# Kernel tuning notes

Hardware: AMD Instinct MI355X
Metric: run time of the kernel (lower is better)

Reference implementation:

```python
import jax, jax.numpy as jnp
import numpy as np

N = 32768        # nodes
E = 524288       # edges (avg in-degree 16)
G = 256          # graphs in batch (128 nodes each)
D = 64           # hidden_dim
DE = 64          # edge_dim
L = 4            # PNA layers
ATOM, BOND = 32, 8
AVG_D_LOG = float(np.log(17.0))   # avg_d['log'] for avg degree 16
EPS = 1e-5


def setup_inputs() -> dict:
    key = jax.random.key(0)
    ks = jax.random.split(key, 16)
    h_tok = jax.random.randint(ks[0], (N,), 0, ATOM, dtype=jnp.int32)
    e_tok = jax.random.randint(ks[1], (E,), 0, BOND, dtype=jnp.int32)
    src = jax.random.randint(ks[2], (E,), 0, N, dtype=jnp.int32)
    dst = jax.random.randint(ks[3], (E,), 0, N, dtype=jnp.int32)
    graph_id = (jnp.arange(N, dtype=jnp.int32) // (N // G)).astype(jnp.int32)
    snorm_n = jnp.full((N, 1), 1.0 / np.sqrt(N // G), dtype=jnp.float32)
    s = 0.05
    emb_h = s * jax.random.normal(ks[4], (ATOM, D), dtype=jnp.float32)
    emb_e = s * jax.random.normal(ks[5], (BOND, DE), dtype=jnp.float32)
    W_pre = s * jax.random.normal(ks[6], (L, 2 * D + DE, D), dtype=jnp.float32)
    b_pre = jnp.zeros((L, D), dtype=jnp.float32)
    W_post = s * jax.random.normal(ks[7], (L, 13 * D, D), dtype=jnp.float32)
    b_post = jnp.zeros((L, D), dtype=jnp.float32)
    bn_gamma = jnp.ones((L, D), dtype=jnp.float32)
    bn_beta = jnp.zeros((L, D), dtype=jnp.float32)
    W1 = s * jax.random.normal(ks[8], (D, D // 2), dtype=jnp.float32)
    b1 = jnp.zeros((D // 2,), dtype=jnp.float32)
    W2 = s * jax.random.normal(ks[9], (D // 2, D // 4), dtype=jnp.float32)
    b2 = jnp.zeros((D // 4,), dtype=jnp.float32)
    W3 = s * jax.random.normal(ks[10], (D // 4, 1), dtype=jnp.float32)
    b3 = jnp.zeros((1,), dtype=jnp.float32)
    return dict(h_tok=h_tok, e_tok=e_tok, src=src, dst=dst, graph_id=graph_id,
                snorm_n=snorm_n, emb_h=emb_h, emb_e=emb_e,
                W_pre=W_pre, b_pre=b_pre, W_post=W_post, b_post=b_post,
                bn_gamma=bn_gamma, bn_beta=bn_beta,
                W1=W1, b1=b1, W2=W2, b2=b2, W3=W3, b3=b3)


def _pna_forward(h_tok, e_tok, src, dst, graph_id, snorm_n, emb_h, emb_e,
                 W_pre, b_pre, W_post, b_post, bn_gamma, bn_beta,
                 W1, b1, W2, b2, W3, b3):
    h = emb_h[h_tok]                     # [N, D] atom embedding (dropout p=0)
    e = emb_e[e_tok]                     # [E, DE] bond embedding
    deg = jax.ops.segment_sum(jnp.ones((E,), h.dtype), dst, num_segments=N)   # in-degree
    deg_safe = jnp.maximum(deg, 1.0)[:, None]
    logd = jnp.log(deg + 1.0)
    amp = (logd / AVG_D_LOG)[:, None]                        # amplification scaler
    att = (AVG_D_LOG / jnp.maximum(logd, 1e-6))[:, None]     # attenuation scaler
    has_nb = (deg > 0)[:, None]

    for l in range(L):
        h_in = h
        # pretrans on (h_src, h_dst, e)
        m_in = jnp.concatenate([h[src], h[dst], e], axis=-1)          # [E, 2D+DE]
        msg = m_in @ W_pre[l] + b_pre[l]                              # [E, D]
        s1 = jax.ops.segment_sum(msg, dst, num_segments=N)
        s2 = jax.ops.segment_sum(msg * msg, dst, num_segments=N)
        mean = s1 / deg_safe
        std = jnp.sqrt(jax.nn.relu(s2 / deg_safe - mean * mean) + EPS)
        mx = jnp.where(has_nb, jax.ops.segment_max(msg, dst, num_segments=N), 0.0)
        mn = jnp.where(has_nb, jax.ops.segment_min(msg, dst, num_segments=N), 0.0)
        agg = jnp.concatenate([mean, mx, mn, std], axis=-1)           # [N, 4D]
        agg = jnp.concatenate([agg, agg * amp, agg * att], axis=-1)   # [N, 12D]
        # posttrans on (h, aggregated)
        h = jnp.concatenate([h, agg], axis=-1) @ W_post[l] + b_post[l]  # [N, D]
        h = h * snorm_n                                               # graph norm
        mu = jnp.mean(h, axis=0)                                      # batchnorm (train mode)
        var = jnp.var(h, axis=0)
        h = bn_gamma[l] * (h - mu) * jax.lax.rsqrt(var + EPS) + bn_beta[l]
        h = jax.nn.relu(h)
        h = h + h_in                                                  # residual

    # mean-nodes readout per graph
    cnt = jax.ops.segment_sum(jnp.ones((N,), h.dtype), graph_id, num_segments=G)
    hg = jax.ops.segment_sum(h, graph_id, num_segments=G) / jnp.maximum(cnt, 1.0)[:, None]
    # MLPReadout: D -> D/2 -> D/4 -> 1
    out = jax.nn.relu(hg @ W1 + b1)
    out = jax.nn.relu(out @ W2 + b2)
    return out @ W3 + b3                                              # [G, 1]


def reference(h_tok, e_tok, src, dst, graph_id, snorm_n, emb_h, emb_e,
              W_pre, b_pre, W_post, b_post, bn_gamma, bn_beta,
              W1, b1, W2, b2, W3, b3):
    return _pna_forward(h_tok, e_tok, src, dst, graph_id, snorm_n, emb_h, emb_e,
                        W_pre, b_pre, W_post, b_post, bn_gamma, bn_beta,
                        W1, b1, W2, b2, W3, b3)
```

## Files before the change

kernel.cpp:

```cpp
#include <hip/hip_runtime.h>
#include <math.h>
#include <float.h>

#define NN 32768
#define NE 524288
#define NG 256
#define DD 64
#define NL 4
#define AVGDLOG 2.8332133340562162f
#define BN_EPS 1e-5f

typedef __attribute__((ext_vector_type(8))) short bf16x8;
typedef __attribute__((ext_vector_type(4))) float f32x4;

static __device__ __forceinline__ unsigned int f2bf_pack(float lo, float hi) {
    unsigned int ulo = __float_as_uint(lo);
    unsigned int uhi = __float_as_uint(hi);
    ulo = ulo + 0x7FFFu + ((ulo >> 16) & 1u);
    uhi = uhi + 0x7FFFu + ((uhi >> 16) & 1u);
    return (ulo >> 16) | (uhi & 0xFFFF0000u);
}
static __device__ __forceinline__ unsigned short f2bf1(float x) {
    unsigned int u = __float_as_uint(x);
    u = u + 0x7FFFu + ((u >> 16) & 1u);
    return (unsigned short)(u >> 16);
}
static __device__ __forceinline__ float bf2f(unsigned short s) {
    return __uint_as_float((unsigned int)s << 16);
}


__global__ void k_deg(const int* __restrict__ dst, int* __restrict__ deg) {
    int e = blockIdx.x * 256 + threadIdx.x;
    if (e < NE) atomicAdd(&deg[dst[e]], 1);
}

__global__ __launch_bounds__(1024) void k_scan(const int* __restrict__ deg,
                                               int* __restrict__ row_start,
                                               int* __restrict__ cursor,
                                               float* __restrict__ amp,
                                               float* __restrict__ att,
                                               float* __restrict__ invdeg) {
    __shared__ int sd[1024];
    int t = threadIdx.x;
    int base = t * 32;
    int loc[32];
    int s = 0;
#pragma unroll
    for (int i = 0; i < 32; i++) { loc[i] = deg[base + i]; s += loc[i]; }
    sd[t] = s;
    __syncthreads();
    for (int off = 1; off < 1024; off <<= 1) {
        int v = (t >= off) ? sd[t - off] : 0;
        __syncthreads();
        sd[t] += v;
        __syncthreads();
    }
    int run = sd[t] - s;
#pragma unroll
    for (int i = 0; i < 32; i++) {
        int idx = base + i;
        row_start[idx] = run;
        cursor[idx] = run;
        int dg = loc[i];
        float d = (float)dg;
        float logd = logf(d + 1.0f);
        amp[idx] = logd * (1.0f / AVGDLOG);
        att[idx] = AVGDLOG / fmaxf(logd, 1e-6f);
        invdeg[idx] = 1.0f / fmaxf(d, 1.0f);
        run += dg;
    }
    if (t == 1023) row_start[NN] = run;
}

__global__ void k_scatter(const int* __restrict__ src, const int* __restrict__ dst,
                          const int* __restrict__ e_tok, int* __restrict__ cursor,
                          int* __restrict__ csr) {
    int e = blockIdx.x * 256 + threadIdx.x;
    int d = dst[e];
    int p = atomicAdd(&cursor[d], 1);
    csr[p] = (src[e] << 3) | (e_tok[e] & 7);
}

__global__ void k_bond(const float* __restrict__ emb_e, const float* __restrict__ W_pre,
                       const float* __restrict__ b_pre, float* __restrict__ bond) {
    int t = blockIdx.x * 256 + threadIdx.x;
    int j = t & 63, r = (t >> 6) & 7, l = t >> 9;
    float s = b_pre[l * DD + j];
    const float* w = W_pre + (size_t)l * 192 * DD + 128 * DD + j;
    const float* e = emb_e + r * DD;
#pragma unroll
    for (int k = 0; k < DD; k++) s = fmaf(e[k], w[k * DD], s);
    bond[t] = s;
}

__global__ __launch_bounds__(256) void k_wprep(const float* __restrict__ W_post,
                                               unsigned short* __restrict__ wt_hi) {
    int b = blockIdx.x;
    int t = threadIdx.x;
    int l = b / 192;
    int j = b - l * 192;
    int c = j >> 6, jj = j & 63;
    float wv = W_post[((size_t)l * 832 + 64 + c * 256 + t) * 64 + jj];
    wt_hi[((size_t)b << 8) + t] = f2bf1(wv);
}


#define FMA4(acc, a, wv) \
    acc.x = fmaf(a, wv.x, acc.x); acc.y = fmaf(a, wv.y, acc.y); \
    acc.z = fmaf(a, wv.z, acc.z); acc.w = fmaf(a, wv.w, acc.w);

__global__ __launch_bounds__(256) void k_A(const int* __restrict__ h_tok,
                                           const float* __restrict__ emb_h,
                                           const float* __restrict__ h_pre,
                                           float* __restrict__ h_cur,
                                           const float* __restrict__ bn_acc,
                                           const float* __restrict__ gamma,
                                           const float* __restrict__ beta,
                                           const float* __restrict__ W_pre,
                                           const float* __restrict__ W_post, int l,
                                           unsigned short* __restrict__ tsb,
                                           float* __restrict__ td,
                                           float* __restrict__ base_o) {
    __shared__ float wl[3 * 4096];
    __shared__ float hl[64 * 68];
    int t = threadIdx.x;
    int j0 = (t & 15) << 2;
    int q4 = (t >> 4) << 2;
    int n0 = blockIdx.x * 64;
    const float* W0 = W_pre + (size_t)l * 192 * DD;
    const float* W1 = W0 + 64 * DD;
    const float* W2 = W_post + (size_t)l * 832 * DD;
#pragma unroll
    for (int s = 0; s < 12; ++s) {
        int g = s * 256 + t;
        int c = g >> 10;
        int k = (g >> 4) & 63;
        int c4 = (g & 15) << 2;
        const float* Wc = (c == 0) ? W0 : (c == 1 ? W1 : W2);
        *(float4*)&wl[c * 4096 + k * 64 + c4] = *(const float4*)&Wc[(size_t)k * 64 + c4];
    }
    if (l == 0) {
#pragma unroll
        for (int s = 0; s < 4; ++s) {
            int g = s * 256 + t;
            int row = g >> 4;
            int tok = h_tok[n0 + row];
            float4 v = *(const float4*)&emb_h[(size_t)tok * DD + j0];
            *(float4*)&hl[row * 68 + j0] = v;
            *(float4*)&h_cur[(size_t)(n0 + row) * DD + j0] = v;
        }
    } else {
        int lp = l - 1;
        float mu0, mu1, mu2, mu3, iv0, iv1, iv2, iv3;
        float ga0, ga1, ga2, ga3, be0, be1, be2, be3;
#define BNPAR(I, MU, IV, GA, BE) { \
        float m_ = bn_acc[lp * 128 + j0 + I] * (1.0f / NN); \
        float v_ = bn_acc[lp * 128 + 64 + j0 + I] * (1.0f / NN) - m_ * m_; \
        MU = m_; IV = rsqrtf(v_ + BN_EPS); \
        GA = gamma[lp * DD + j0 + I]; BE = beta[lp * DD + j0 + I]; }
        BNPAR(0, mu0, iv0, ga0, be0)
        BNPAR(1, mu1, iv1, ga1, be1)
        BNPAR(2, mu2, iv2, ga2, be2)
        BNPAR(3, mu3, iv3, ga3, be3)
#undef BNPAR
#pragma unroll
        for (int s = 0; s < 4; ++s) {
            int g = s * 256 + t;
            int row = g >> 4;
            size_t gb = (size_t)(n0 + row) * DD + j0;
            float4 hp = *(const float4*)&h_pre[gb];
            float4 hc = *(const float4*)&h_cur[gb];
            float4 v;
            v.x = hc.x + fmaxf(ga0 * (hp.x - mu0) * iv0 + be0, 0.f);
            v.y = hc.y + fmaxf(ga1 * (hp.y - mu1) * iv1 + be1, 0.f);
            v.z = hc.z + fmaxf(ga2 * (hp.z - mu2) * iv2 + be2, 0.f);
            v.w = hc.w + fmaxf(ga3 * (hp.w - mu3) * iv3 + be3, 0.f);
            *(float4*)&hl[row * 68 + j0] = v;
            *(float4*)&h_cur[gb] = v;
        }
    }
    __syncthreads();
    float4 z4 = make_float4(0.f, 0.f, 0.f, 0.f);
    float4 c0_0 = z4, c0_1 = z4, c0_2 = z4, c0_3 = z4;
    float4 c1_0 = z4, c1_1 = z4, c1_2 = z4, c1_3 = z4;
    float4 c2_0 = z4, c2_1 = z4, c2_2 = z4, c2_3 = z4;
#pragma unroll
    for (int k4 = 0; k4 < 16; ++k4) {
        int ab = k4 << 2;
        float4 av0 = *(const float4*)&hl[(q4 + 0) * 68 + ab];
        float4 av1 = *(const float4*)&hl[(q4 + 1) * 68 + ab];
        float4 av2 = *(const float4*)&hl[(q4 + 2) * 68 + ab];
        float4 av3 = *(const float4*)&hl[(q4 + 3) * 68 + ab];
#define ASTEP(KK, COMP) { \
        int widx = (ab + KK) * 64 + j0; \
        float4 wv0 = *(const float4*)&wl[widx]; \
        float4 wv1 = *(const float4*)&wl[4096 + widx]; \
        float4 wv2 = *(const float4*)&wl[8192 + widx]; \
        FMA4(c0_0, av0.COMP, wv0) FMA4(c1_0, av0.COMP, wv1) FMA4(c2_0, av0.COMP, wv2) \
        FMA4(c0_1, av1.COMP, wv0) FMA4(c1_1, av1.COMP, wv1) FMA4(c2_1, av1.COMP, wv2) \
        FMA4(c0_2, av2.COMP, wv0) FMA4(c1_2, av2.COMP, wv1) FMA4(c2_2, av2.COMP, wv2) \
        FMA4(c0_3, av3.COMP, wv0) FMA4(c1_3, av3.COMP, wv1) FMA4(c2_3, av3.COMP, wv2) }
        ASTEP(0, x) ASTEP(1, y) ASTEP(2, z) ASTEP(3, w)
#undef ASTEP
    }
#define AOUT(I, A0, A1, A2) { \
    size_t n = (size_t)(n0 + q4 + I); \
    uint2 pk; \
    pk.x = f2bf_pack(A0.x, A0.y); \
    pk.y = f2bf_pack(A0.z, A0.w); \
    *(uint2*)&tsb[n * DD + j0] = pk; \
    *(float4*)&td[n * DD + j0] = A1; \
    *(float4*)&base_o[n * DD + j0] = A2; }
    AOUT(0, c0_0, c1_0, c2_0)
    AOUT(1, c0_1, c1_1, c2_1)
    AOUT(2, c0_2, c1_2, c2_2)
    AOUT(3, c0_3, c1_3, c2_3)
#undef AOUT
}

__global__ __launch_bounds__(256) void k_B(const unsigned short* __restrict__ tsb,
                                           const float* __restrict__ td,
                                           const float* __restrict__ bond_l,
                                           const int* __restrict__ row_start,
                                           const int* __restrict__ csr,
                                           const float* __restrict__ invdeg,
                                           unsigned short* __restrict__ agg_b) {
    int t = threadIdx.x;
    int lane = t & 63;
    int q = __builtin_amdgcn_readfirstlane(t >> 6);
    int n = blockIdx.x * 4 + q;
    int rs = __builtin_amdgcn_readfirstlane(row_start[n]);
    int re = __builtin_amdgcn_readfirstlane(row_start[n + 1]);
    int cnt = re - rs;
    const int* cp = csr + rs;
    float tdv = td[(size_t)n * DD + lane];
    float s1 = 0.f, s2 = 0.f, mx = -FLT_MAX, mn = FLT_MAX;
    int i = 0;
    for (; i + 8 <= cnt; i += 8) {
        int p[8];
#pragma unroll
        for (int u = 0; u < 8; ++u) p[u] = cp[i + u];
        unsigned short r_[8];
#pragma unroll
        for (int u = 0; u < 8; ++u) r_[u] = tsb[(size_t)(p[u] >> 3) * DD + lane];
        float m[8];
#pragma unroll
        for (int u = 0; u < 8; ++u) m[u] = bf2f(r_[u]) + bond_l[((p[u] & 7) << 6) + lane] + tdv;
#pragma unroll
        for (int u = 0; u < 8; ++u) {
            s1 += m[u]; s2 = fmaf(m[u], m[u], s2);
            mx = fmaxf(mx, m[u]); mn = fminf(mn, m[u]);
        }
    }
    for (; i < cnt; i++) {
        int p0 = cp[i];
        float m0 = bf2f(tsb[(size_t)(p0 >> 3) * DD + lane]) + bond_l[((p0 & 7) << 6) + lane] + tdv;
        s1 += m0; s2 = fmaf(m0, m0, s2); mx = fmaxf(mx, m0); mn = fminf(mn, m0);
    }
    float iv = invdeg[n];
    float mean = s1 * iv;
    float var = fmaxf(s2 * iv - mean * mean, 0.f);
    float sd = sqrtf(var + BN_EPS);
    bool has = cnt > 0;
    mx = has ? mx : 0.f;
    mn = has ? mn : 0.f;
    unsigned short* ao = agg_b + (size_t)n * 256;
    ao[lane] = f2bf1(mean);
    ao[64 + lane] = f2bf1(mx);
    ao[128 + lane] = f2bf1(mn);
    ao[192 + lane] = f2bf1(sd);
}

__global__ __launch_bounds__(256) void k_C(const unsigned short* __restrict__ agg_b,
                                           const float* __restrict__ base_i,
                                           const unsigned short* __restrict__ wt_hi,
                                           const float* __restrict__ b_post, int l,
                                           const float* __restrict__ amp,
                                           const float* __restrict__ att,
                                           const float* __restrict__ snorm,
                                           float* __restrict__ h_pre,
                                           float* __restrict__ bn_acc) {
    __shared__ short whl[192 * 40];
    __shared__ short agl[64 * 40];
    int t = threadIdx.x;
    int lane = t & 63;
    int w = t >> 6;
    int rA = lane & 15;
    int kg8 = (lane >> 4) << 3;
    int n0 = blockIdx.x * 64;
    const unsigned short* whg = wt_hi + ((size_t)l * 192 << 8);
    f32x4 dz = {0.f, 0.f, 0.f, 0.f};
    f32x4 d[12];
#pragma unroll
    for (int i = 0; i < 12; ++i) d[i] = dz;

    for (int kc = 0; kc < 8; ++kc) {
        if (kc) __syncthreads();
#pragma unroll
        for (int s = 0; s < 3; ++s) {
            int q = s * 256 + t;
            int j = q >> 2, k8 = (q & 3) << 3;
            *(float4*)&whl[j * 40 + k8] =
                *(const float4*)&whg[((size_t)j << 8) + kc * 32 + k8];
        }
        {
            int n = t >> 2, k8 = (t & 3) << 3;
            *(float4*)&agl[n * 40 + k8] =
                *(const float4*)&agg_b[(size_t)(n0 + n) * 256 + kc * 32 + k8];
        }
        __syncthreads();
        bf16x8 af = *(const bf16x8*)&agl[(w * 16 + rA) * 40 + kg8];
#pragma unroll
        for (int ct = 0; ct < 12; ++ct) {
            bf16x8 bh = *(const bf16x8*)&whl[(ct * 16 + rA) * 40 + kg8];
            d[ct] = __builtin_amdgcn_mfma_f32_16x16x32_bf16(af, bh, d[ct], 0, 0, 0);
        }
    }

    int g = lane >> 4;
    float ps0 = 0.f, ps1 = 0.f, ps2 = 0.f, ps3 = 0.f;
    float qs0 = 0.f, qs1 = 0.f, qs2 = 0.f, qs3 = 0.f;
    float bp0 = b_post[l * DD + rA];
    float bp1 = b_post[l * DD + 16 + rA];
    float bp2 = b_post[l * DD + 32 + rA];
    float bp3 = b_post[l * DD + 48 + rA];
#pragma unroll
    for (int i = 0; i < 4; ++i) {
        int n = n0 + w * 16 + g * 4 + i;
        float am = amp[n], at2 = att[n], sn = snorm[n];
        size_t nb = (size_t)n * DD;
#define CEP(CT, BP, PS, QS) { \
        int j = CT * 16 + rA; \
        float o = (base_i[nb + j] + BP + d[CT][i] + am * d[CT + 4][i] + at2 * d[CT + 8][i]) * sn; \
        h_pre[nb + j] = o; \
        PS += o; QS = fmaf(o, o, QS); }
        CEP(0, bp0, ps0, qs0)
        CEP(1, bp1, ps1, qs1)
        CEP(2, bp2, ps2, qs2)
        CEP(3, bp3, ps3, qs3)
#undef CEP
    }
    __syncthreads();
    float* red = (float*)whl;
    int slot = (w << 2) + g;
    red[(rA) * 16 + slot] = ps0;
    red[(16 + rA) * 16 + slot] = ps1;
    red[(32 + rA) * 16 + slot] = ps2;
    red[(48 + rA) * 16 + slot] = ps3;
    red[1024 + (rA) * 16 + slot] = qs0;
    red[1024 + (16 + rA) * 16 + slot] = qs1;
    red[1024 + (32 + rA) * 16 + slot] = qs2;
    red[1024 + (48 + rA) * 16 + slot] = qs3;
    __syncthreads();
    if (t < 64) {
        float s = 0.f, s2 = 0.f;
#pragma unroll
        for (int u = 0; u < 16; ++u) {
            s += red[t * 16 + u];
            s2 += red[1024 + t * 16 + u];
        }
        atomicAdd(&bn_acc[l * 128 + t], s);
        atomicAdd(&bn_acc[l * 128 + 64 + t], s2);
    }
}

__global__ __launch_bounds__(256) void k_read(const float* __restrict__ h_pre,
                                              const float* __restrict__ h_cur,
                                              const float* __restrict__ bn_acc,
                                              const float* __restrict__ gamma,
                                              const float* __restrict__ beta,
                                              const float* __restrict__ W1, const float* __restrict__ b1,
                                              const float* __restrict__ W2, const float* __restrict__ b2,
                                              const float* __restrict__ W3, const float* __restrict__ b3,
                                              float* __restrict__ out) {
    __shared__ float red[256];
    __shared__ float hgs[64];
    __shared__ float o1[32];
    __shared__ float o2[16];
    int g = blockIdx.x, t = threadIdx.x;
    int lane = t & 63, w = t >> 6;
    int lp = NL - 1;
    float mu = bn_acc[lp * 128 + lane] * (1.0f / NN);
    float va = bn_acc[lp * 128 + 64 + lane] * (1.0f / NN) - mu * mu;
    float iv = rsqrtf(va + BN_EPS);
    float ga = gamma[lp * DD + lane], be = beta[lp * DD + lane];
    float acc = 0.f;
    for (int i = w * 32; i < w * 32 + 32; i++) {
        size_t idx = (size_t)(g * 128 + i) * DD + lane;
        float v = h_cur[idx] + fmaxf(ga * (h_pre[idx] - mu) * iv + be, 0.f);
        acc += v;
    }
    red[w * 64 + lane] = acc;
    __syncthreads();
    if (t < 64) {
        hgs[t] = (red[t] + red[64 + t] + red[128 + t] + red[192 + t]) * (1.0f / 128.0f);
    }
    __syncthreads();
    if (t < 32) {
        float s = b1[t];
#pragma unroll
        for (int k = 0; k < 64; k++) s = fmaf(hgs[k], W1[k * 32 + t], s);
        o1[t] = fmaxf(s, 0.f);
    }
    __syncthreads();
    if (t < 16) {
        float s = b2[t];
#pragma unroll
        for (int k = 0; k < 32; k++) s = fmaf(o1[k], W2[k * 16 + t], s);
        o2[t] = fmaxf(s, 0.f);
    }
    __syncthreads();
    if (t == 0) {
        float s = b3[0];
#pragma unroll
        for (int k = 0; k < 16; k++) s = fmaf(o2[k], W3[k], s);
        out[g] = s;
    }
}


extern "C" void kernel_launch(void* const* d_in, const int* in_sizes, int n_in,
                              void* d_out, int out_size, void* d_ws, size_t ws_size,
                              hipStream_t stream) {
    const int* h_tok = (const int*)d_in[0];
    const int* e_tok = (const int*)d_in[1];
    const int* src = (const int*)d_in[2];
    const int* dst = (const int*)d_in[3];
    const float* snorm = (const float*)d_in[5];
    const float* emb_h = (const float*)d_in[6];
    const float* emb_e = (const float*)d_in[7];
    const float* W_pre = (const float*)d_in[8];
    const float* b_pre = (const float*)d_in[9];
    const float* W_post = (const float*)d_in[10];
    const float* b_post = (const float*)d_in[11];
    const float* gamma = (const float*)d_in[12];
    const float* beta = (const float*)d_in[13];
    const float* W1 = (const float*)d_in[14];
    const float* b1 = (const float*)d_in[15];
    const float* W2 = (const float*)d_in[16];
    const float* b2 = (const float*)d_in[17];
    const float* W3 = (const float*)d_in[18];
    const float* b3 = (const float*)d_in[19];
    float* out = (float*)d_out;

    char* ws = (char*)d_ws;
    size_t off = 0;
    auto alloc = [&](size_t bytes) {
        void* p = ws + off;
        off += (bytes + 255) & ~(size_t)255;
        return p;
    };
    float* h_cur = (float*)alloc((size_t)NN * DD * 4);
    float* h_pre = (float*)alloc((size_t)NN * DD * 4);
    unsigned short* tsb = (unsigned short*)alloc((size_t)NN * DD * 2);
    float* td = (float*)alloc((size_t)NN * DD * 4);
    float* base_b = (float*)alloc((size_t)NN * DD * 4);
    unsigned short* agg_b = (unsigned short*)alloc((size_t)NN * 256 * 2);
    unsigned short* wt_hi = (unsigned short*)alloc((size_t)NL * 192 * 256 * 2);
    int* deg = (int*)alloc((size_t)NN * 4);
    int* row_start = (int*)alloc((size_t)(NN + 1) * 4);
    int* cursor = (int*)alloc((size_t)NN * 4);
    int* csr = (int*)alloc((size_t)NE * 4);
    float* amp = (float*)alloc((size_t)NN * 4);
    float* att = (float*)alloc((size_t)NN * 4);
    float* invdeg = (float*)alloc((size_t)NN * 4);
    float* bond = (float*)alloc((size_t)NL * 8 * DD * 4);
    float* bn_acc = (float*)alloc((size_t)NL * 128 * 4);

    hipMemsetAsync(deg, 0, (size_t)NN * 4, stream);
    hipMemsetAsync(bn_acc, 0, (size_t)NL * 128 * 4, stream);

    k_deg<<<NE / 256, 256, 0, stream>>>(dst, deg);
    k_scan<<<1, 1024, 0, stream>>>(deg, row_start, cursor, amp, att, invdeg);
    k_scatter<<<NE / 256, 256, 0, stream>>>(src, dst, e_tok, cursor, csr);
    k_bond<<<NL * 8 * DD / 256, 256, 0, stream>>>(emb_e, W_pre, b_pre, bond);
    k_wprep<<<NL * 192, 256, 0, stream>>>(W_post, wt_hi);

    for (int l = 0; l < NL; l++) {
        k_A<<<NN / 64, 256, 0, stream>>>(h_tok, emb_h, h_pre, h_cur, bn_acc, gamma, beta,
                                         W_pre, W_post, l, tsb, td, base_b);
        k_B<<<NN / 4, 256, 0, stream>>>(tsb, td, bond + l * 8 * DD, row_start, csr, invdeg, agg_b);
        k_C<<<NN / 64, 256, 0, stream>>>(agg_b, base_b, wt_hi, b_post, l, amp, att,
                                         snorm, h_pre, bn_acc);
    }
    k_read<<<NG, 256, 0, stream>>>(h_pre, h_cur, bn_acc, gamma, beta,
                                   W1, b1, W2, b2, W3, b3, out);
}
```

Measured before the change: 338.2 us.

## Use bf16 MFMA for per-node pre-transform GEMM in k_A with prepacked weights

```diff
diff --git a/kernel.cpp b/kernel.cpp
--- a/kernel.cpp
+++ b/kernel.cpp
@@ -105,10 +105,21 @@
     wt_hi[((size_t)b << 8) + t] = f2bf1(wv);
 }
 
-
-#define FMA4(acc, a, wv) \
-    acc.x = fmaf(a, wv.x, acc.x); acc.y = fmaf(a, wv.y, acc.y); \
-    acc.z = fmaf(a, wv.z, acc.z); acc.w = fmaf(a, wv.w, acc.w);
+__global__ __launch_bounds__(64) void k_waprep(const float* __restrict__ W_pre,
+                                               const float* __restrict__ W_post,
+                                               unsigned short* __restrict__ wa) {
+    int b = blockIdx.x;
+    int t = threadIdx.x;
+    int l = b / 192;
+    int j = b - l * 192;
+    int c = j >> 6, jj = j & 63;
+    float wv;
+    if (c == 0)      wv = W_pre[((size_t)l * 192 + t) * 64 + jj];
+    else if (c == 1) wv = W_pre[((size_t)l * 192 + 64 + t) * 64 + jj];
+    else             wv = W_post[((size_t)l * 832 + t) * 64 + jj];
+    wa[((size_t)b << 6) + t] = f2bf1(wv);
+}
+
 
 __global__ __launch_bounds__(256) void k_A(const int* __restrict__ h_tok,
                                            const float* __restrict__ emb_h,
@@ -117,38 +128,40 @@
                                            const float* __restrict__ bn_acc,
                                            const float* __restrict__ gamma,
                                            const float* __restrict__ beta,
-                                           const float* __restrict__ W_pre,
-                                           const float* __restrict__ W_post, int l,
+                                           const unsigned short* __restrict__ wa, int l,
                                            unsigned short* __restrict__ tsb,
                                            float* __restrict__ td,
                                            float* __restrict__ base_o) {
-    __shared__ float wl[3 * 4096];
-    __shared__ float hl[64 * 68];
-    int t = threadIdx.x;
+    __shared__ short whl[2][192 * 40];
+    __shared__ short ahl[2][64 * 40];
+    int t = threadIdx.x;
+    int lane = t & 63;
+    int w = t >> 6;
+    int rA = lane & 15;
+    int kg8 = (lane >> 4) << 3;
     int j0 = (t & 15) << 2;
-    int q4 = (t >> 4) << 2;
+    int pa = j0 >> 5, ko = j0 & 31;
     int n0 = blockIdx.x * 64;
-    const float* W0 = W_pre + (size_t)l * 192 * DD;
-    const float* W1 = W0 + 64 * DD;
-    const float* W2 = W_post + (size_t)l * 832 * DD;
-#pragma unroll
-    for (int s = 0; s < 12; ++s) {
-        int g = s * 256 + t;
-        int c = g >> 10;
-        int k = (g >> 4) & 63;
-        int c4 = (g & 15) << 2;
-        const float* Wc = (c == 0) ? W0 : (c == 1 ? W1 : W2);
-        *(float4*)&wl[c * 4096 + k * 64 + c4] = *(const float4*)&Wc[(size_t)k * 64 + c4];
+    const unsigned short* wag = wa + ((size_t)l * 192 << 6);
+#pragma unroll
+    for (int s = 0; s < 6; ++s) {
+        int u = s * 256 + t;
+        int j = u >> 3, k8 = (u & 7) << 3;
+        *(float4*)&whl[k8 >> 5][j * 40 + (k8 & 31)] =
+            *(const float4*)&wag[((size_t)j << 6) + k8];
     }
     if (l == 0) {
 #pragma unroll
         for (int s = 0; s < 4; ++s) {
-            int g = s * 256 + t;
-            int row = g >> 4;
+            int gg = s * 256 + t;
+            int row = gg >> 4;
             int tok = h_tok[n0 + row];
             float4 v = *(const float4*)&emb_h[(size_t)tok * DD + j0];
-            *(float4*)&hl[row * 68 + j0] = v;
             *(float4*)&h_cur[(size_t)(n0 + row) * DD + j0] = v;
+            uint2 pk;
+            pk.x = f2bf_pack(v.x, v.y);
+            pk.y = f2bf_pack(v.z, v.w);
+            *(uint2*)&ahl[pa][row * 40 + ko] = pk;
         }
     } else {
         int lp = l - 1;
@@ -166,8 +179,8 @@
 #undef BNPAR
 #pragma unroll
         for (int s = 0; s < 4; ++s) {
-            int g = s * 256 + t;
-            int row = g >> 4;
+            int gg = s * 256 + t;
+            int row = gg >> 4;
             size_t gb = (size_t)(n0 + row) * DD + j0;
             float4 hp = *(const float4*)&h_pre[gb];
             float4 hc = *(const float4*)&h_cur[gb];
@@ -176,47 +189,41 @@
             v.y = hc.y + fmaxf(ga1 * (hp.y - mu1) * iv1 + be1, 0.f);
             v.z = hc.z + fmaxf(ga2 * (hp.z - mu2) * iv2 + be2, 0.f);
             v.w = hc.w + fmaxf(ga3 * (hp.w - mu3) * iv3 + be3, 0.f);
-            *(float4*)&hl[row * 68 + j0] = v;
             *(float4*)&h_cur[gb] = v;
-        }
-    }
-    __syncthreads();
-    float4 z4 = make_float4(0.f, 0.f, 0.f, 0.f);
-    float4 c0_0 = z4, c0_1 = z4, c0_2 = z4, c0_3 = z4;
-    float4 c1_0 = z4, c1_1 = z4, c1_2 = z4, c1_3 = z4;
-    float4 c2_0 = z4, c2_1 = z4, c2_2 = z4, c2_3 = z4;
-#pragma unroll
-    for (int k4 = 0; k4 < 16; ++k4) {
-        int ab = k4 << 2;
-        float4 av0 = *(const float4*)&hl[(q4 + 0) * 68 + ab];
-        float4 av1 = *(const float4*)&hl[(q4 + 1) * 68 + ab];
-        float4 av2 = *(const float4*)&hl[(q4 + 2) * 68 + ab];
-        float4 av3 = *(const float4*)&hl[(q4 + 3) * 68 + ab];
-#define ASTEP(KK, COMP) { \
-        int widx = (ab + KK) * 64 + j0; \
-        float4 wv0 = *(const float4*)&wl[widx]; \
-        float4 wv1 = *(const float4*)&wl[4096 + widx]; \
-        float4 wv2 = *(const float4*)&wl[8192 + widx]; \
-        FMA4(c0_0, av0.COMP, wv0) FMA4(c1_0, av0.COMP, wv1) FMA4(c2_0, av0.COMP, wv2) \
-        FMA4(c0_1, av1.COMP, wv0) FMA4(c1_1, av1.COMP, wv1) FMA4(c2_1, av1.COMP, wv2) \
-        FMA4(c0_2, av2.COMP, wv0) FMA4(c1_2, av2.COMP, wv1) FMA4(c2_2, av2.COMP, wv2) \
-        FMA4(c0_3, av3.COMP, wv0) FMA4(c1_3, av3.COMP, wv1) FMA4(c2_3, av3.COMP, wv2) }
-        ASTEP(0, x) ASTEP(1, y) ASTEP(2, z) ASTEP(3, w)
-#undef ASTEP
-    }
-#define AOUT(I, A0, A1, A2) { \
-    size_t n = (size_t)(n0 + q4 + I); \
-    uint2 pk; \
-    pk.x = f2bf_pack(A0.x, A0.y); \
-    pk.y = f2bf_pack(A0.z, A0.w); \
-    *(uint2*)&tsb[n * DD + j0] = pk; \
-    *(float4*)&td[n * DD + j0] = A1; \
-    *(float4*)&base_o[n * DD + j0] = A2; }
-    AOUT(0, c0_0, c1_0, c2_0)
-    AOUT(1, c0_1, c1_1, c2_1)
-    AOUT(2, c0_2, c1_2, c2_2)
-    AOUT(3, c0_3, c1_3, c2_3)
-#undef AOUT
+            uint2 pk;
+            pk.x = f2bf_pack(v.x, v.y);
+            pk.y = f2bf_pack(v.z, v.w);
+            *(uint2*)&ahl[pa][row * 40 + ko] = pk;
+        }
+    }
+    __syncthreads();
+    f32x4 dz = {0.f, 0.f, 0.f, 0.f};
+    f32x4 d[12];
+#pragma unroll
+    for (int i = 0; i < 12; ++i) d[i] = dz;
+    bf16x8 af0 = *(const bf16x8*)&ahl[0][(w * 16 + rA) * 40 + kg8];
+    bf16x8 af1 = *(const bf16x8*)&ahl[1][(w * 16 + rA) * 40 + kg8];
+#pragma unroll
+    for (int ct = 0; ct < 12; ++ct) {
+        bf16x8 b0 = *(const bf16x8*)&whl[0][(ct * 16 + rA) * 40 + kg8];
+        bf16x8 b1 = *(const bf16x8*)&whl[1][(ct * 16 + rA) * 40 + kg8];
+        d[ct] = __builtin_amdgcn_mfma_f32_16x16x32_bf16(af0, b0, d[ct], 0, 0, 0);
+        d[ct] = __builtin_amdgcn_mfma_f32_16x16x32_bf16(af1, b1, d[ct], 0, 0, 0);
+    }
+    int g = lane >> 4;
+#pragma unroll
+    for (int i = 0; i < 4; ++i) {
+        size_t nb = (size_t)(n0 + w * 16 + g * 4 + i) * DD;
+#pragma unroll
+        for (int ct = 0; ct < 4; ++ct)
+            tsb[nb + ct * 16 + rA] = f2bf1(d[ct][i]);
+#pragma unroll
+        for (int ct = 0; ct < 4; ++ct)
+            td[nb + ct * 16 + rA] = d[ct + 4][i];
+#pragma unroll
+        for (int ct = 0; ct < 4; ++ct)
+            base_o[nb + ct * 16 + rA] = d[ct + 8][i];
+    }
 }
 
 __global__ __launch_bounds__(256) void k_B(const unsigned short* __restrict__ tsb,
@@ -458,6 +465,7 @@
     float* base_b = (float*)alloc((size_t)NN * DD * 4);
     unsigned short* agg_b = (unsigned short*)alloc((size_t)NN * 256 * 2);
     unsigned short* wt_hi = (unsigned short*)alloc((size_t)NL * 192 * 256 * 2);
+    unsigned short* wa = (unsigned short*)alloc((size_t)NL * 192 * 64 * 2);
     int* deg = (int*)alloc((size_t)NN * 4);
     int* row_start = (int*)alloc((size_t)(NN + 1) * 4);
     int* cursor = (int*)alloc((size_t)NN * 4);
@@ -476,10 +484,11 @@
     k_scatter<<<NE / 256, 256, 0, stream>>>(src, dst, e_tok, cursor, csr);
     k_bond<<<NL * 8 * DD / 256, 256, 0, stream>>>(emb_e, W_pre, b_pre, bond);
     k_wprep<<<NL * 192, 256, 0, stream>>>(W_post, wt_hi);
+    k_waprep<<<NL * 192, 64, 0, stream>>>(W_pre, W_post, wa);
 
     for (int l = 0; l < NL; l++) {
         k_A<<<NN / 64, 256, 0, stream>>>(h_tok, emb_h, h_pre, h_cur, bn_acc, gamma, beta,
-                                         W_pre, W_post, l, tsb, td, base_b);
+                                         wa, l, tsb, td, base_b);
         k_B<<<NN / 4, 256, 0, stream>>>(tsb, td, bond + l * 8 * DD, row_start, csr, invdeg, agg_b);
         k_C<<<NN / 64, 256, 0, stream>>>(agg_b, base_b, wt_hi, b_post, l, amp, att,
                                          snorm, h_pre, bn_acc);
```

Result: faster. 313.2 us (-7.4%).
